# Optimization experiments

Measured on AMD Instinct MI355X. Metric: run time of the kernel, lower is better.

The kernel has to match this reference:

```python
import jax, jax.numpy as jnp
import numpy as np

E, M, K, I, TOPK = 8, 4096, 2048, 1408, 2
N = 2 * I  # gated: w1 produces [gate, up]


def setup_inputs() -> dict:
    key = jax.random.key(0)
    k1, k2, k3, k4, k5 = jax.random.split(key, 5)
    hidden_states = jax.random.normal(k1, (M, K), dtype=jnp.float32)
    w1 = jax.random.normal(k2, (E, N, K), dtype=jnp.float32) * 0.02
    w2 = jax.random.normal(k3, (E, K, I), dtype=jnp.float32) * 0.02
    raw = jax.random.uniform(k4, (M, TOPK), dtype=jnp.float32)
    topk_weights = raw / jnp.sum(raw, axis=-1, keepdims=True)  # router probs
    topk_ids = jax.random.randint(k5, (M, TOPK), 0, E, dtype=jnp.int32)
    return {
        "hidden_states": hidden_states,
        "w1": w1,
        "w2": w2,
        "topk_weights": topk_weights,
        "topk_ids": topk_ids,
    }


def reference(hidden_states, w1, w2, topk_weights, topk_ids):
    # MoE: permute -> grouped GEMM1 -> silu_and_mul -> grouped GEMM2 -> unpermute+reduce.
    # Dense-per-expert formulation (math-equivalent to grouped GEMM over routed tokens).
    # GEMM1: [E, M, N]
    h1 = jnp.einsum("mk,enk->emn", hidden_states, w1)
    gate, up = h1[..., :I], h1[..., I:]
    act = jax.nn.silu(gate) * up  # silu_and_mul, [E, M, I]
    # GEMM2: [E, M, K]
    y = jnp.einsum("emi,eki->emk", act, w2)
    # Unpermute: gather each token's topk expert outputs, apply router weights, reduce.
    y_tok = jnp.transpose(y, (1, 0, 2))  # [M, E, K]
    sel = jnp.take_along_axis(y_tok, topk_ids[:, :, None].astype(jnp.int32), axis=1)  # [M, topk, K]
    out = jnp.sum(sel * topk_weights[:, :, None], axis=1)  # [M, K]
    return out
```

## Files before the change

kernel.cpp:

```cpp
#include <hip/hip_runtime.h>
#include <hip/hip_bf16.h>
#include <stdint.h>

#define EXPERTS 8
#define MTOK 4096
#define KDIM 2048
#define IDIM 1408
#define NDIM 2816
#define CAP  8192

typedef __attribute__((ext_vector_type(8))) short bf16x8;
typedef __attribute__((ext_vector_type(4))) float f32x4;

__device__ __forceinline__ unsigned short f2bf(float x) {
    unsigned u = __float_as_uint(x);
    u = u + 0x7fffu + ((u >> 16) & 1u);
    return (unsigned short)(u >> 16);
}

__device__ __forceinline__ bf16x8 cvt8(float4 x, float4 y) {
    bf16x8 r;
    r[0] = (short)f2bf(x.x); r[1] = (short)f2bf(x.y);
    r[2] = (short)f2bf(x.z); r[3] = (short)f2bf(x.w);
    r[4] = (short)f2bf(y.x); r[5] = (short)f2bf(y.y);
    r[6] = (short)f2bf(y.z); r[7] = (short)f2bf(y.w);
    return r;
}

__device__ __forceinline__ void gload16(const void* g, void* l) {
    __builtin_amdgcn_global_load_lds(
        (const __attribute__((address_space(1))) void*)g,
        (__attribute__((address_space(3))) void*)l, 16, 0, 0);
}

__global__ void __launch_bounds__(256) conv_bf16(const float* __restrict__ src,
                                                 unsigned short* __restrict__ dst, int n4) {
    int i = blockIdx.x * 256 + threadIdx.x;
    int st = gridDim.x * 256;
    for (; i < n4; i += st) {
        float4 v = reinterpret_cast<const float4*>(src)[i];
        ushort4 r;
        r.x = f2bf(v.x); r.y = f2bf(v.y); r.z = f2bf(v.z); r.w = f2bf(v.w);
        reinterpret_cast<ushort4*>(dst)[i] = r;
    }
}

__global__ void __launch_bounds__(256) router(const float* __restrict__ tw,
                                              const int* __restrict__ ids,
                                              int* __restrict__ tok, float* __restrict__ wgt,
                                              int* __restrict__ cnt) {
    int m = blockIdx.x * 256 + threadIdx.x;
    if (m >= MTOK) return;
#pragma unroll
    for (int t = 0; t < 2; t++) {
        int e = ids[m * 2 + t];
        int slot = atomicAdd(&cnt[e], 1);
        tok[e * CAP + slot] = m;
        wgt[e * CAP + slot] = tw[m * 2 + t];
    }
}

__global__ void scan_off(const int* __restrict__ cnt, int* __restrict__ off) {
    if (threadIdx.x == 0) {
        int s = 0;
        for (int e = 0; e < EXPERTS; e++) { off[e] = s; s += cnt[e]; }
    }
}

__global__ void __launch_bounds__(256) pack_a(const float* __restrict__ hs,
                                              const int* __restrict__ tok,
                                              const int* __restrict__ off,
                                              unsigned short* __restrict__ hsp) {
    const int slot = blockIdx.x * 8 + (threadIdx.x >> 5);
    const int lane = threadIdx.x & 31;
    int e = 0;
#pragma unroll
    for (int k = 1; k < 8; k++) if (slot >= off[k]) e = k;
    const int idx = slot - off[e];
    const int row = tok[e * CAP + idx];
    const float* src = hs + (size_t)row * KDIM;
    unsigned short* dst = hsp + (size_t)slot * KDIM;
#pragma unroll
    for (int i = 0; i < 8; i++) {
        int c = (i * 32 + lane) * 8;
        float4 x = *(const float4*)(src + c);
        float4 y = *(const float4*)(src + c + 4);
        *(bf16x8*)(dst + c) = cvt8(x, y);
    }
}


__global__ void __launch_bounds__(256, 3) gemm1_silu(
    const unsigned short* __restrict__ hsp,
    const unsigned short* __restrict__ w1b,
    const int* __restrict__ cnt,
    const int* __restrict__ off,
    unsigned short* __restrict__ act) {
    const int bid = blockIdx.x;
    const int e = bid & 7;
    const int j = bid >> 3;
    const int rb = j & 63;
    const int cb = j >> 6;
    const int cnt_e = cnt[e];
    if (rb * 128 >= cnt_e) return;
    const int off_e = off[e];
    const int slotA = off_e + rb * 128;
    const int NT = KDIM / 32;

    __shared__ __align__(16) char smem[49152];

    const int tid = threadIdx.x;
    const int w = tid >> 6, lane = tid & 63;

    const int o0 = w * 1024 + lane * 16;
    const int row0 = o0 >> 6, g0 = ((o0 >> 4) & 3) ^ ((row0 >> 1) & 3);
    const int o1 = 4096 + o0;
    const int row1 = o1 >> 6, g1 = ((o1 >> 4) & 3) ^ ((row1 >> 1) & 3);

    const int G0 = row0 >> 4, G1 = row1 >> 4;
    const size_t w1base = (size_t)e * NDIM * KDIM;
    const int wrow0 = ((G0 & 1) ? IDIM : 0) + cb * 64 + (G0 >> 1) * 16 + (row0 & 15);
    const int wrow1 = ((G1 & 1) ? IDIM : 0) + cb * 64 + (G1 >> 1) * 16 + (row1 & 15);

    const size_t srcA0 = (size_t)(slotA + row0) * KDIM + g0 * 8;
    const size_t srcA1 = (size_t)(slotA + row1) * KDIM + g1 * 8;
    const size_t srcB0 = w1base + (size_t)wrow0 * KDIM + g0 * 8;
    const size_t srcB1 = w1base + (size_t)wrow1 * KDIM + g1 * 8;

    const int wr = w >> 1, wc = w & 1;
    const int l16 = lane & 15, lg = lane >> 4;
    int aoff[4], boff[4];
#pragma unroll
    for (int m = 0; m < 4; m++) {
        int r = wr * 64 + m * 16 + l16;
        aoff[m] = r * 64 + ((lg ^ ((r >> 1) & 3)) * 16);
    }
#pragma unroll
    for (int n = 0; n < 4; n++) {
        int r = wc * 64 + n * 16 + l16;
        boff[n] = 8192 + r * 64 + ((lg ^ ((r >> 1) & 3)) * 16);
    }

    f32x4 acc[4][4];
#pragma unroll
    for (int m = 0; m < 4; m++)
#pragma unroll
        for (int n = 0; n < 4; n++) acc[m][n] = {0.f, 0.f, 0.f, 0.f};

#define STG1(t, base) { const int kof_ = (t) * 32; char* b_ = smem + (base); \
    gload16(hsp + srcA0 + kof_, b_ + w * 1024); \
    gload16(hsp + srcA1 + kof_, b_ + 4096 + w * 1024); \
    gload16(w1b + srcB0 + kof_, b_ + 8192 + w * 1024); \
    gload16(w1b + srcB1 + kof_, b_ + 12288 + w * 1024); }

    STG1(0, 0); STG1(1, 16384);
    asm volatile("s_waitcnt vmcnt(4)" ::: "memory");
    __builtin_amdgcn_sched_barrier(0);
    __builtin_amdgcn_s_barrier();

    int sl_t = 0;
    int sl_p = 32768;

#pragma unroll 1
    for (int t = 0; t < NT; ++t) {
        if (t + 2 < NT) STG1(t + 2, sl_p);
        __builtin_amdgcn_sched_barrier(0);

        const char* db = smem + sl_t;
        bf16x8 af[4], bf[4];
#pragma unroll
        for (int m = 0; m < 4; m++) af[m] = *(const bf16x8*)(db + aoff[m]);
#pragma unroll
        for (int n = 0; n < 4; n++) bf[n] = *(const bf16x8*)(db + boff[n]);
        __builtin_amdgcn_s_setprio(1);
#pragma unroll
        for (int m = 0; m < 4; m++)
#pragma unroll
            for (int n = 0; n < 4; n++)
                acc[m][n] = __builtin_amdgcn_mfma_f32_16x16x32_bf16(af[m], bf[n], acc[m][n], 0, 0, 0);
        __builtin_amdgcn_s_setprio(0);
        __builtin_amdgcn_sched_barrier(0);
        if (t + 2 < NT)      { asm volatile("s_waitcnt vmcnt(4)" ::: "memory"); }
        else if (t + 1 < NT) { asm volatile("s_waitcnt vmcnt(0)" ::: "memory"); }
        __builtin_amdgcn_sched_barrier(0);
        __builtin_amdgcn_s_barrier();

        sl_t += 16384; if (sl_t == 49152) sl_t = 0;
        sl_p += 16384; if (sl_p == 49152) sl_p = 0;
    }
#undef STG1

#pragma unroll
    for (int m = 0; m < 4; m++) {
#pragma unroll
        for (int np = 0; np < 2; np++) {
            f32x4 g4 = acc[m][np * 2];
            f32x4 u4 = acc[m][np * 2 + 1];
            int icol = cb * 64 + (wc * 2 + np) * 16 + l16;
#pragma unroll
            for (int j2 = 0; j2 < 4; j2++) {
                int grow = rb * 128 + wr * 64 + m * 16 + lg * 4 + j2;
                if (grow < cnt_e) {
                    float gt = g4[j2], up = u4[j2];
                    float s = gt / (1.f + __expf(-gt));
                    act[(size_t)(off_e + grow) * IDIM + icol] = f2bf(s * up);
                }
            }
        }
    }
}

__global__ void __launch_bounds__(256, 3) gemm2_scatter(
    const unsigned short* __restrict__ act,
    const unsigned short* __restrict__ w2b,
    const int* __restrict__ tok,
    const float* __restrict__ wgt,
    const int* __restrict__ cnt,
    const int* __restrict__ off,
    float* __restrict__ out) {
    const int bid = blockIdx.x;
    const int e = bid & 7;
    const int j = bid >> 3;
    const int rb = j & 63;
    const int cb = j >> 6;
    const int cnt_e = cnt[e];
    if (rb * 128 >= cnt_e) return;
    const int off_e = off[e];
    const int NT = IDIM / 32;

    __shared__ __align__(16) char smem[49152];
    __shared__ int toks[128];
    __shared__ float wgts[128];

    const int tid = threadIdx.x;
    const int w = tid >> 6, lane = tid & 63;
    if (tid < 128) {
        int slot = rb * 128 + tid;
        bool v = slot < cnt_e;
        toks[tid] = v ? tok[e * CAP + slot] : 0;
        wgts[tid] = v ? wgt[e * CAP + slot] : 0.f;
    }
    __syncthreads();

    const int o0 = w * 1024 + lane * 16;
    const int row0 = o0 >> 6, g0 = ((o0 >> 4) & 3) ^ ((row0 >> 1) & 3);
    const int o1 = 4096 + o0;
    const int row1 = o1 >> 6, g1 = ((o1 >> 4) & 3) ^ ((row1 >> 1) & 3);

    const int s0 = rb * 128 + row0, s1 = rb * 128 + row1;
    const size_t pa0 = (size_t)(off_e + (s0 < cnt_e ? s0 : 0)) * IDIM + g0 * 8;
    const size_t pa1 = (size_t)(off_e + (s1 < cnt_e ? s1 : 0)) * IDIM + g1 * 8;
    const size_t w2base = (size_t)e * KDIM * IDIM;
    const size_t pb0 = w2base + (size_t)(cb * 128 + row0) * IDIM + g0 * 8;
    const size_t pb1 = w2base + (size_t)(cb * 128 + row1) * IDIM + g1 * 8;

    const int wr = w >> 1, wc = w & 1;
    const int l16 = lane & 15, lg = lane >> 4;
    int aoff[4], boff[4];
#pragma unroll
    for (int m = 0; m < 4; m++) {
        int r = wr * 64 + m * 16 + l16;
        aoff[m] = r * 64 + ((lg ^ ((r >> 1) & 3)) * 16);
    }
#pragma unroll
    for (int n = 0; n < 4; n++) {
        int r = wc * 64 + n * 16 + l16;
        boff[n] = 8192 + r * 64 + ((lg ^ ((r >> 1) & 3)) * 16);
    }

    f32x4 acc[4][4];
#pragma unroll
    for (int m = 0; m < 4; m++)
#pragma unroll
        for (int n = 0; n < 4; n++) acc[m][n] = {0.f, 0.f, 0.f, 0.f};

#define STG2(t, base) { const int kof_ = (t) * 32; char* b_ = smem + (base); \
    gload16(act + pa0 + kof_, b_ + w * 1024); \
    gload16(act + pa1 + kof_, b_ + 4096 + w * 1024); \
    gload16(w2b + pb0 + kof_, b_ + 8192 + w * 1024); \
    gload16(w2b + pb1 + kof_, b_ + 12288 + w * 1024); }

    STG2(0, 0); STG2(1, 16384);
    asm volatile("s_waitcnt vmcnt(4)" ::: "memory");
    __builtin_amdgcn_sched_barrier(0);
    __builtin_amdgcn_s_barrier();

    int sl_t = 0;
    int sl_p = 32768;

#pragma unroll 1
    for (int t = 0; t < NT; ++t) {
        if (t + 2 < NT) STG2(t + 2, sl_p);
        __builtin_amdgcn_sched_barrier(0);

        const char* db = smem + sl_t;
        bf16x8 af[4], bf[4];
#pragma unroll
        for (int m = 0; m < 4; m++) af[m] = *(const bf16x8*)(db + aoff[m]);
#pragma unroll
        for (int n = 0; n < 4; n++) bf[n] = *(const bf16x8*)(db + boff[n]);
        __builtin_amdgcn_s_setprio(1);
#pragma unroll
        for (int m = 0; m < 4; m++)
#pragma unroll
            for (int n = 0; n < 4; n++)
                acc[m][n] = __builtin_amdgcn_mfma_f32_16x16x32_bf16(af[m], bf[n], acc[m][n], 0, 0, 0);
        __builtin_amdgcn_s_setprio(0);
        __builtin_amdgcn_sched_barrier(0);
        if (t + 2 < NT)      { asm volatile("s_waitcnt vmcnt(4)" ::: "memory"); }
        else if (t + 1 < NT) { asm volatile("s_waitcnt vmcnt(0)" ::: "memory"); }
        __builtin_amdgcn_sched_barrier(0);
        __builtin_amdgcn_s_barrier();

        sl_t += 16384; if (sl_t == 49152) sl_t = 0;
        sl_p += 16384; if (sl_p == 49152) sl_p = 0;
    }
#undef STG2

#pragma unroll
    for (int m = 0; m < 4; m++) {
#pragma unroll
        for (int n = 0; n < 4; n++) {
            int kcol = cb * 128 + wc * 64 + n * 16 + l16;
#pragma unroll
            for (int j2 = 0; j2 < 4; j2++) {
                int lrow = wr * 64 + m * 16 + lg * 4 + j2;
                if (rb * 128 + lrow < cnt_e) {
                    atomicAdd(&out[(size_t)toks[lrow] * KDIM + kcol],
                              wgts[lrow] * acc[m][n][j2]);
                }
            }
        }
    }
}

extern "C" void kernel_launch(void* const* d_in, const int* in_sizes, int n_in,
                              void* d_out, int out_size, void* d_ws, size_t ws_size,
                              hipStream_t stream) {
    const float* hs  = (const float*)d_in[0];
    const float* w1  = (const float*)d_in[1];
    const float* w2  = (const float*)d_in[2];
    const float* tw  = (const float*)d_in[3];
    const int*   ids = (const int*)d_in[4];
    float* out = (float*)d_out;

    char* ws = (char*)d_ws;
    unsigned short* w1b  = (unsigned short*)(ws);
    unsigned short* hsp  = (unsigned short*)(ws + 92274688ull);
    unsigned short* w2b  = (unsigned short*)(ws + 92274688ull);
    unsigned short* actb = (unsigned short*)(ws + 138412032ull);
    int*   tokb = (int*)  (ws + 161480704ull);
    float* wgtb = (float*)(ws + 161742848ull);
    int*   cntb = (int*)  (ws + 162004992ull);
    int*   offb = (int*)  (ws + 162005056ull);

    hipMemsetAsync(d_out, 0, (size_t)MTOK * KDIM * sizeof(float), stream);
    hipMemsetAsync(cntb, 0, 64, stream);

    conv_bf16<<<4096, 256, 0, stream>>>(w1, w1b, EXPERTS * NDIM * KDIM / 4);

    router<<<MTOK / 256, 256, 0, stream>>>(tw, ids, tokb, wgtb, cntb);
    scan_off<<<1, 64, 0, stream>>>(cntb, offb);
    pack_a<<<MTOK * 2 / 8, 256, 0, stream>>>(hs, tokb, offb, hsp);

    gemm1_silu<<<dim3(22 * 64 * 8, 1, 1), 256, 0, stream>>>(hsp, w1b, cntb, offb, actb);

    conv_bf16<<<2048, 256, 0, stream>>>(w2, w2b, EXPERTS * KDIM * IDIM / 4);

    gemm2_scatter<<<dim3(16 * 64 * 8, 1, 1), 256, 0, stream>>>(actb, w2b, tokb, wgtb, cntb, offb, out);
}
```

Before: 395.2 us.

## Fuse w2 fp32-to-bf16 conversion into GEMM2 loads via register staging

Removes the separate conv_bf16 pass over w2. GEMM2 now loads fp32 weight rows straight into registers, converts them to bf16 and writes them into shared memory, with two register sets ping-ponging inside a loop unrolled by two. This avoids writing and re-reading a bf16 copy of w2 in memory. In exchange, every GEMM2 block reads fp32 weights (twice the bytes, repeated across row blocks), uses more registers and adds conversion work inside the main loop. Workspace offsets are compacted to match.

Result: no change. 397.7 us (+0.6%).

```diff
diff --git a/kernel.cpp b/kernel.cpp
--- a/kernel.cpp
+++ b/kernel.cpp
@@ -212,7 +212,7 @@
 
 __global__ void __launch_bounds__(256, 3) gemm2_scatter(
     const unsigned short* __restrict__ act,
-    const unsigned short* __restrict__ w2b,
+    const float* __restrict__ w2,
     const int* __restrict__ tok,
     const float* __restrict__ wgt,
     const int* __restrict__ cnt,
@@ -274,48 +274,73 @@
 #pragma unroll
         for (int n = 0; n < 4; n++) acc[m][n] = {0.f, 0.f, 0.f, 0.f};
 
-#define STG2(t, base) { const int kof_ = (t) * 32; char* b_ = smem + (base); \
+    struct BReg { float4 x0, y0, x1, y1; };
+    BReg RbA, RbB;
+
+#define ISSUE2(t, base, R) { const int kof_ = (t) * 32; char* b_ = smem + (base); \
     gload16(act + pa0 + kof_, b_ + w * 1024); \
     gload16(act + pa1 + kof_, b_ + 4096 + w * 1024); \
-    gload16(w2b + pb0 + kof_, b_ + 8192 + w * 1024); \
-    gload16(w2b + pb1 + kof_, b_ + 12288 + w * 1024); }
-
-    STG2(0, 0); STG2(1, 16384);
-    asm volatile("s_waitcnt vmcnt(4)" ::: "memory");
+    R.x0 = *(const float4*)(w2 + pb0 + kof_); R.y0 = *(const float4*)(w2 + pb0 + kof_ + 4); \
+    R.x1 = *(const float4*)(w2 + pb1 + kof_); R.y1 = *(const float4*)(w2 + pb1 + kof_ + 4); }
+#define WRITEB2(R, base) { char* b_ = smem + (base); \
+    *(bf16x8*)(b_ + 8192 + o0) = cvt8(R.x0, R.y0); \
+    *(bf16x8*)(b_ + 8192 + o1) = cvt8(R.x1, R.y1); }
+#define COMPUTE2(base) { const char* db = smem + (base); bf16x8 af[4], bf[4]; \
+    _Pragma("unroll") for (int m = 0; m < 4; m++) af[m] = *(const bf16x8*)(db + aoff[m]); \
+    _Pragma("unroll") for (int n = 0; n < 4; n++) bf[n] = *(const bf16x8*)(db + boff[n]); \
+    __builtin_amdgcn_s_setprio(1); \
+    _Pragma("unroll") for (int m = 0; m < 4; m++) \
+    _Pragma("unroll") for (int n = 0; n < 4; n++) \
+        acc[m][n] = __builtin_amdgcn_mfma_f32_16x16x32_bf16(af[m], bf[n], acc[m][n], 0, 0, 0); \
+    __builtin_amdgcn_s_setprio(0); }
+
+    ISSUE2(0, 0, RbA);
+    ISSUE2(1, 16384, RbB);
+    asm volatile("s_waitcnt vmcnt(6)" ::: "memory");
+    __builtin_amdgcn_sched_barrier(0);
+    WRITEB2(RbA, 0);
+    asm volatile("s_waitcnt lgkmcnt(0)" ::: "memory");
     __builtin_amdgcn_sched_barrier(0);
     __builtin_amdgcn_s_barrier();
 
-    int sl_t = 0;
-    int sl_p = 32768;
+    int sl0 = 0, sl1 = 16384, sl2 = 32768;
 
 #pragma unroll 1
-    for (int t = 0; t < NT; ++t) {
-        if (t + 2 < NT) STG2(t + 2, sl_p);
-        __builtin_amdgcn_sched_barrier(0);
-
-        const char* db = smem + sl_t;
-        bf16x8 af[4], bf[4];
-#pragma unroll
-        for (int m = 0; m < 4; m++) af[m] = *(const bf16x8*)(db + aoff[m]);
-#pragma unroll
-        for (int n = 0; n < 4; n++) bf[n] = *(const bf16x8*)(db + boff[n]);
-        __builtin_amdgcn_s_setprio(1);
-#pragma unroll
-        for (int m = 0; m < 4; m++)
-#pragma unroll
-            for (int n = 0; n < 4; n++)
-                acc[m][n] = __builtin_amdgcn_mfma_f32_16x16x32_bf16(af[m], bf[n], acc[m][n], 0, 0, 0);
-        __builtin_amdgcn_s_setprio(0);
-        __builtin_amdgcn_sched_barrier(0);
-        if (t + 2 < NT)      { asm volatile("s_waitcnt vmcnt(4)" ::: "memory"); }
-        else if (t + 1 < NT) { asm volatile("s_waitcnt vmcnt(0)" ::: "memory"); }
-        __builtin_amdgcn_sched_barrier(0);
-        __builtin_amdgcn_s_barrier();
-
-        sl_t += 16384; if (sl_t == 49152) sl_t = 0;
-        sl_p += 16384; if (sl_p == 49152) sl_p = 0;
-    }
-#undef STG2
+    for (int t = 0; t < NT; t += 2) {
+        if (t + 2 < NT) ISSUE2(t + 2, sl2, RbA);
+        __builtin_amdgcn_sched_barrier(0);
+        COMPUTE2(sl0);
+        __builtin_amdgcn_sched_barrier(0);
+        if (t + 1 < NT) {
+            if (t + 2 < NT) { asm volatile("s_waitcnt vmcnt(6)" ::: "memory"); }
+            else            { asm volatile("s_waitcnt vmcnt(0)" ::: "memory"); }
+            __builtin_amdgcn_sched_barrier(0);
+            WRITEB2(RbB, sl1);
+            asm volatile("s_waitcnt lgkmcnt(0)" ::: "memory");
+            __builtin_amdgcn_sched_barrier(0);
+            __builtin_amdgcn_s_barrier();
+        }
+        { int tmp = sl0; sl0 = sl1; sl1 = sl2; sl2 = tmp; }
+
+        if (t + 1 >= NT) break;
+        if (t + 3 < NT) ISSUE2(t + 3, sl2, RbB);
+        __builtin_amdgcn_sched_barrier(0);
+        COMPUTE2(sl0);
+        __builtin_amdgcn_sched_barrier(0);
+        if (t + 2 < NT) {
+            if (t + 3 < NT) { asm volatile("s_waitcnt vmcnt(6)" ::: "memory"); }
+            else            { asm volatile("s_waitcnt vmcnt(0)" ::: "memory"); }
+            __builtin_amdgcn_sched_barrier(0);
+            WRITEB2(RbA, sl1);
+            asm volatile("s_waitcnt lgkmcnt(0)" ::: "memory");
+            __builtin_amdgcn_sched_barrier(0);
+            __builtin_amdgcn_s_barrier();
+        }
+        { int tmp = sl0; sl0 = sl1; sl1 = sl2; sl2 = tmp; }
+    }
+#undef ISSUE2
+#undef WRITEB2
+#undef COMPUTE2
 
 #pragma unroll
     for (int m = 0; m < 4; m++) {
@@ -347,12 +372,11 @@
     char* ws = (char*)d_ws;
     unsigned short* w1b  = (unsigned short*)(ws);
     unsigned short* hsp  = (unsigned short*)(ws + 92274688ull);
-    unsigned short* w2b  = (unsigned short*)(ws + 92274688ull);
-    unsigned short* actb = (unsigned short*)(ws + 138412032ull);
-    int*   tokb = (int*)  (ws + 161480704ull);
-    float* wgtb = (float*)(ws + 161742848ull);
-    int*   cntb = (int*)  (ws + 162004992ull);
-    int*   offb = (int*)  (ws + 162005056ull);
+    unsigned short* actb = (unsigned short*)(ws + 126353408ull);
+    int*   tokb = (int*)  (ws + 149422080ull);
+    float* wgtb = (float*)(ws + 149684224ull);
+    int*   cntb = (int*)  (ws + 149946368ull);
+    int*   offb = (int*)  (ws + 149946432ull);
 
     hipMemsetAsync(d_out, 0, (size_t)MTOK * KDIM * sizeof(float), stream);
     hipMemsetAsync(cntb, 0, 64, stream);
@@ -364,8 +388,5 @@
     pack_a<<<MTOK * 2 / 8, 256, 0, stream>>>(hs, tokb, offb, hsp);
 
     gemm1_silu<<<dim3(22 * 64 * 8, 1, 1), 256, 0, stream>>>(hsp, w1b, cntb, offb, actb);
-
-    conv_bf16<<<2048, 256, 0, stream>>>(w2, w2b, EXPERTS * KDIM * IDIM / 4);
-
-    gemm2_scatter<<<dim3(16 * 64 * 8, 1, 1), 256, 0, stream>>>(actb, w2b, tokb, wgtb, cntb, offb, out);
-}
+    gemm2_scatter<<<dim3(16 * 64 * 8, 1, 1), 256, 0, stream>>>(actb, w2, tokb, wgtb, cntb, offb, out);
+}
```
